# Optimization experiments

Measured on AMD Instinct MI355X. Metric: run time of the kernel, lower is better.

The kernel has to match this reference:

```python
import math
import jax, jax.numpy as jnp
import numpy as np

HEAD_DIM = 64

def setup_inputs() -> dict:
    key = jax.random.key(0)
    kq, kk, kv = jax.random.split(key, 3)
    B, S, D = 16, 2048, HEAD_DIM
    q = jax.random.normal(kq, (B, S, D), dtype=jnp.float32)
    k = jax.random.normal(kk, (B, S, D), dtype=jnp.float32)
    v = jax.random.normal(kv, (B, S, D), dtype=jnp.float32)
    return {"q": q, "k": k, "v": v}

def reference(q, k, v):
    # scores: [B, Sq, Sk]
    scores = jnp.einsum('bqd,bkd->bqk', q, k) / math.sqrt(HEAD_DIM)
    # NOTE: original uses nn.Softmax(dim=1) -> softmax over the QUERY axis
    weights = jax.nn.softmax(scores, axis=1)
    # dropout p=0.0 -> identity
    return jnp.einsum('bqk,bkd->bqd', weights, v)
```

## Files before the change

kernel.cpp:

```cpp
#include <hip/hip_runtime.h>
#include <hip/hip_bf16.h>

#define S_LEN 2048
#define D_DIM 64
#define NB 16

#define C_EXP 0.1803368801111204f

typedef __attribute__((ext_vector_type(8))) __bf16 bf16x8;
typedef __attribute__((ext_vector_type(4))) __bf16 bf16x4;
typedef __attribute__((ext_vector_type(4))) float f32x4;

#define GLOAD16(gp, lp)                                              \
  __builtin_amdgcn_global_load_lds(                                  \
      (const __attribute__((address_space(1))) void*)(gp),           \
      (__attribute__((address_space(3))) void*)(lp), 16, 0, 0)

__global__ __launch_bounds__(256) void convert_bf16_kernel(
    const float* __restrict__ qf, const float* __restrict__ kf,
    __bf16* __restrict__ qb, __bf16* __restrict__ kb) {
  const int n4 = NB * S_LEN * D_DIM / 4;
  for (int i = blockIdx.x * blockDim.x + threadIdx.x; i < n4;
       i += gridDim.x * blockDim.x) {
    float4 a = ((const float4*)qf)[i];
    float4 c = ((const float4*)kf)[i];
    bf16x4 oa = {(__bf16)a.x, (__bf16)a.y, (__bf16)a.z, (__bf16)a.w};
    bf16x4 oc = {(__bf16)c.x, (__bf16)c.y, (__bf16)c.z, (__bf16)c.w};
    ((bf16x4*)qb)[i] = oa;
    ((bf16x4*)kb)[i] = oc;
  }
}

__global__ __launch_bounds__(256) void stats_kernel(
    const __bf16* __restrict__ Qb, const __bf16* __restrict__ Kb,
    float* __restrict__ Lpart, int qlen) {
  __shared__ __align__(16) __bf16 QT[4096];
  const int b = blockIdx.y;
  const int kblk = blockIdx.x;
  const int qs = blockIdx.z;
  const int tid = threadIdx.x;
  const int wave = tid >> 6;
  const int lane = tid & 63;
  const int l16 = lane & 15;
  const int g = lane >> 4;

  const int kbase = kblk * 64 + wave * 16;
  const __bf16* kp = Kb + ((size_t)b * S_LEN + kbase + l16) * D_DIM + g * 8;
  bf16x8 ak0 = *(const bf16x8*)(kp);
  bf16x8 ak1 = *(const bf16x8*)(kp + 32);

  const int srow = tid >> 3;
  const int scol = 8 * ((tid & 7) ^ (srow & 7));

  float sacc[4] = {0.f, 0.f, 0.f, 0.f};
  const __bf16* Qbase = Qb + (size_t)b * S_LEN * D_DIM;
  const int qbeg = qs * qlen;

  for (int q0 = qbeg; q0 < qbeg + qlen; q0 += 64) {
    __syncthreads();
#pragma unroll
    for (int h = 0; h < 2; ++h)
      GLOAD16(Qbase + (size_t)(q0 + h * 32 + srow) * D_DIM + scol,
              (char*)QT + h * 4096 + (size_t)tid * 16);
    asm volatile("s_waitcnt vmcnt(0)" ::: "memory");
    __syncthreads();

#pragma unroll
    for (int qt = 0; qt < 4; ++qt) {
      const int r = qt * 16 + l16;
      bf16x8 bq0 = *(const bf16x8*)(QT + r * 64 + 8 * (g ^ (r & 7)));
      bf16x8 bq1 = *(const bf16x8*)(QT + r * 64 + 8 * ((g + 4) ^ (r & 7)));
      f32x4 t = __builtin_amdgcn_mfma_f32_16x16x32_bf16(
          ak0, bq0, (f32x4){0.f, 0.f, 0.f, 0.f}, 0, 0, 0);
      t = __builtin_amdgcn_mfma_f32_16x16x32_bf16(ak1, bq1, t, 0, 0, 0);
#pragma unroll
      for (int r4 = 0; r4 < 4; ++r4)
        sacc[r4] += __builtin_amdgcn_exp2f(t[r4] * C_EXP);
    }
  }
#pragma unroll
  for (int r4 = 0; r4 < 4; ++r4) {
    float v = sacc[r4];
    v += __shfl_xor(v, 1);
    v += __shfl_xor(v, 2);
    v += __shfl_xor(v, 4);
    v += __shfl_xor(v, 8);
    if (l16 == 0)
      Lpart[(size_t)qs * NB * S_LEN + (size_t)b * S_LEN + kbase + g * 4 + r4] =
          v;
  }
}

__global__ __launch_bounds__(256) void scalev_kernel(
    const float* __restrict__ V, const float* __restrict__ Lpart,
    __bf16* __restrict__ Vt) {
  const int b = blockIdx.y;
  const int k = blockIdx.x * 256 + threadIdx.x;
  const size_t NS = (size_t)NB * S_LEN;
  const size_t idx = (size_t)b * S_LEN + k;
  const float L =
      Lpart[idx] + Lpart[NS + idx] + Lpart[2 * NS + idx] + Lpart[3 * NS + idx];
  const float inv = 1.0f / L;
  const float* vrow = V + ((size_t)b * S_LEN + k) * D_DIM;
  __bf16* vt = Vt + (size_t)b * D_DIM * S_LEN + k;
#pragma unroll
  for (int d = 0; d < D_DIM; ++d)
    vt[(size_t)d * S_LEN] = (__bf16)(vrow[d] * inv);
}

__global__ __launch_bounds__(256) void attn_out_kernel(
    const __bf16* __restrict__ Qb, const __bf16* __restrict__ Kb,
    const __bf16* __restrict__ Vt, float* __restrict__ Op, int klen) {
  __shared__ __align__(16) __bf16 KT[4096];
  __shared__ __align__(16) __bf16 VT[4096];
  __shared__ __align__(16) __bf16 Plds[4][16][72];
  const int b = blockIdx.y;
  const int qblk = blockIdx.x;
  const int ks = blockIdx.z;
  const int tid = threadIdx.x;
  const int wave = tid >> 6;
  const int lane = tid & 63;
  const int l16 = lane & 15;
  const int g = lane >> 4;

  const int qbase = qblk * 64 + wave * 16;
  const __bf16* qp = Qb + ((size_t)b * S_LEN + qbase + l16) * D_DIM + g * 8;
  bf16x8 aq0 = *(const bf16x8*)(qp);
  bf16x8 aq1 = *(const bf16x8*)(qp + 32);

  f32x4 acc[4] = {};
  const int srow = tid >> 3;
  const int scol = 8 * ((tid & 7) ^ (srow & 7));
  const __bf16* Kbase = Kb + (size_t)b * S_LEN * D_DIM;
  const __bf16* Vbase = Vt + (size_t)b * D_DIM * S_LEN;
  __bf16(*pl)[72] = Plds[wave];
  const int kbeg = ks * klen;

  for (int k0 = kbeg; k0 < kbeg + klen; k0 += 64) {
    __syncthreads();
#pragma unroll
    for (int h = 0; h < 2; ++h) {
      GLOAD16(Kbase + (size_t)(k0 + h * 32 + srow) * D_DIM + scol,
              (char*)KT + h * 4096 + (size_t)tid * 16);
      GLOAD16(Vbase + (size_t)(h * 32 + srow) * S_LEN + k0 + scol,
              (char*)VT + h * 4096 + (size_t)tid * 16);
    }
    asm volatile("s_waitcnt vmcnt(0)" ::: "memory");
    __syncthreads();

#pragma unroll
    for (int kt = 0; kt < 4; ++kt) {
      const int r = kt * 16 + l16;
      bf16x8 bk0 = *(const bf16x8*)(KT + r * 64 + 8 * (g ^ (r & 7)));
      bf16x8 bk1 = *(const bf16x8*)(KT + r * 64 + 8 * ((g + 4) ^ (r & 7)));
      f32x4 t = __builtin_amdgcn_mfma_f32_16x16x32_bf16(
          aq0, bk0, (f32x4){0.f, 0.f, 0.f, 0.f}, 0, 0, 0);
      t = __builtin_amdgcn_mfma_f32_16x16x32_bf16(aq1, bk1, t, 0, 0, 0);
#pragma unroll
      for (int r4 = 0; r4 < 4; ++r4)
        pl[g * 4 + r4][kt * 16 + l16] =
            (__bf16)__builtin_amdgcn_exp2f(t[r4] * C_EXP);
    }
    bf16x8 pa0 = *(const bf16x8*)(&pl[l16][g * 8]);
    bf16x8 pa1 = *(const bf16x8*)(&pl[l16][32 + g * 8]);
#pragma unroll
    for (int dt = 0; dt < 4; ++dt) {
      const int rd = dt * 16 + l16;
      bf16x8 bv0 = *(const bf16x8*)(VT + rd * 64 + 8 * (g ^ (rd & 7)));
      bf16x8 bv1 = *(const bf16x8*)(VT + rd * 64 + 8 * ((g + 4) ^ (rd & 7)));
      acc[dt] = __builtin_amdgcn_mfma_f32_16x16x32_bf16(pa0, bv0, acc[dt], 0, 0, 0);
      acc[dt] = __builtin_amdgcn_mfma_f32_16x16x32_bf16(pa1, bv1, acc[dt], 0, 0, 0);
    }
  }
  float* ob = Op + ((size_t)ks * NB + b) * (size_t)(S_LEN * D_DIM);
#pragma unroll
  for (int dt = 0; dt < 4; ++dt)
#pragma unroll
    for (int r4 = 0; r4 < 4; ++r4)
      ob[(size_t)(qbase + g * 4 + r4) * D_DIM + dt * 16 + l16] = acc[dt][r4];
}

__global__ __launch_bounds__(256) void reduce_kernel(
    const float* __restrict__ Op, float* __restrict__ out, int np) {
  const int i = blockIdx.x * 256 + threadIdx.x;
  const int slab = NB * S_LEN * D_DIM / 4;
  const float4* p = (const float4*)Op;
  float4 s = p[i];
  for (int j = 1; j < np; ++j) {
    float4 t = p[i + (size_t)j * slab];
    s.x += t.x; s.y += t.y; s.z += t.z; s.w += t.w;
  }
  ((float4*)out)[i] = s;
}

extern "C" void kernel_launch(void* const* d_in, const int* in_sizes, int n_in,
                              void* d_out, int out_size, void* d_ws,
                              size_t ws_size, hipStream_t stream) {
  const float* q = (const float*)d_in[0];
  const float* k = (const float*)d_in[1];
  const float* v = (const float*)d_in[2];
  float* out = (float*)d_out;

  char* ws = (char*)d_ws;
  const size_t nelem = (size_t)NB * S_LEN * D_DIM;
  __bf16* Qb = (__bf16*)ws;
  __bf16* Kb = (__bf16*)(ws + nelem * 2);
  __bf16* Vt = (__bf16*)(ws + nelem * 4);
  float* Lp = (float*)(ws + nelem * 6);
  float* Op = (float*)(ws + (13u << 20));

  int ksplit = 1;
  if (ws_size >= (13u << 20) + 4 * nelem * 4) ksplit = 4;
  else if (ws_size >= (13u << 20) + 2 * nelem * 4) ksplit = 2;

  convert_bf16_kernel<<<1024, 256, 0, stream>>>(q, k, Qb, Kb);
  stats_kernel<<<dim3(32, 16, 4), 256, 0, stream>>>(Qb, Kb, Lp, S_LEN / 4);
  scalev_kernel<<<dim3(8, 16), 256, 0, stream>>>(v, Lp, Vt);
  float* attn_dst = (ksplit == 1) ? out : Op;
  attn_out_kernel<<<dim3(32, 16, ksplit), 256, 0, stream>>>(Qb, Kb, Vt,
                                                            attn_dst,
                                                            S_LEN / ksplit);
  if (ksplit > 1)
    reduce_kernel<<<(int)(nelem / 4 / 256), 256, 0, stream>>>(Op, out, ksplit);
}
```

Measured before the change: 134.5 us.

## Load Q/K/V MFMA operands directly from global memory instead of LDS staging

Removes the LDS staging of Q tiles in the stats kernel and K/V tiles in the attention kernel. Each wave now fetches its MFMA B-operands straight from global memory with 16-byte vector loads, which drops the block-wide barriers and the async global-to-LDS copies. The cost is that the four waves of a block each fetch the same K/V/Q data, relying on L1/L2 to absorb the repeats, and load latency is no longer hidden behind an explicit staged tile.

Result: slower. 261.3 us (+94.3%).

```diff
diff --git a/kernel.cpp b/kernel.cpp
--- a/kernel.cpp
+++ b/kernel.cpp
@@ -10,11 +10,6 @@
 typedef __attribute__((ext_vector_type(8))) __bf16 bf16x8;
 typedef __attribute__((ext_vector_type(4))) __bf16 bf16x4;
 typedef __attribute__((ext_vector_type(4))) float f32x4;
-
-#define GLOAD16(gp, lp)                                              \
-  __builtin_amdgcn_global_load_lds(                                  \
-      (const __attribute__((address_space(1))) void*)(gp),           \
-      (__attribute__((address_space(3))) void*)(lp), 16, 0, 0)
 
 __global__ __launch_bounds__(256) void convert_bf16_kernel(
     const float* __restrict__ qf, const float* __restrict__ kf,
@@ -34,13 +29,11 @@
 __global__ __launch_bounds__(256) void stats_kernel(
     const __bf16* __restrict__ Qb, const __bf16* __restrict__ Kb,
     float* __restrict__ Lpart, int qlen) {
-  __shared__ __align__(16) __bf16 QT[4096];
   const int b = blockIdx.y;
   const int kblk = blockIdx.x;
   const int qs = blockIdx.z;
-  const int tid = threadIdx.x;
-  const int wave = tid >> 6;
-  const int lane = tid & 63;
+  const int wave = threadIdx.x >> 6;
+  const int lane = threadIdx.x & 63;
   const int l16 = lane & 15;
   const int g = lane >> 4;
 
@@ -49,27 +42,16 @@
   bf16x8 ak0 = *(const bf16x8*)(kp);
   bf16x8 ak1 = *(const bf16x8*)(kp + 32);
 
-  const int srow = tid >> 3;
-  const int scol = 8 * ((tid & 7) ^ (srow & 7));
-
   float sacc[4] = {0.f, 0.f, 0.f, 0.f};
   const __bf16* Qbase = Qb + (size_t)b * S_LEN * D_DIM;
   const int qbeg = qs * qlen;
 
   for (int q0 = qbeg; q0 < qbeg + qlen; q0 += 64) {
-    __syncthreads();
-#pragma unroll
-    for (int h = 0; h < 2; ++h)
-      GLOAD16(Qbase + (size_t)(q0 + h * 32 + srow) * D_DIM + scol,
-              (char*)QT + h * 4096 + (size_t)tid * 16);
-    asm volatile("s_waitcnt vmcnt(0)" ::: "memory");
-    __syncthreads();
-
 #pragma unroll
     for (int qt = 0; qt < 4; ++qt) {
-      const int r = qt * 16 + l16;
-      bf16x8 bq0 = *(const bf16x8*)(QT + r * 64 + 8 * (g ^ (r & 7)));
-      bf16x8 bq1 = *(const bf16x8*)(QT + r * 64 + 8 * ((g + 4) ^ (r & 7)));
+      const __bf16* qp = Qbase + (size_t)(q0 + qt * 16 + l16) * D_DIM + g * 8;
+      bf16x8 bq0 = *(const bf16x8*)(qp);
+      bf16x8 bq1 = *(const bf16x8*)(qp + 32);
       f32x4 t = __builtin_amdgcn_mfma_f32_16x16x32_bf16(
           ak0, bq0, (f32x4){0.f, 0.f, 0.f, 0.f}, 0, 0, 0);
       t = __builtin_amdgcn_mfma_f32_16x16x32_bf16(ak1, bq1, t, 0, 0, 0);
@@ -111,15 +93,12 @@
 __global__ __launch_bounds__(256) void attn_out_kernel(
     const __bf16* __restrict__ Qb, const __bf16* __restrict__ Kb,
     const __bf16* __restrict__ Vt, float* __restrict__ Op, int klen) {
-  __shared__ __align__(16) __bf16 KT[4096];
-  __shared__ __align__(16) __bf16 VT[4096];
   __shared__ __align__(16) __bf16 Plds[4][16][72];
   const int b = blockIdx.y;
   const int qblk = blockIdx.x;
   const int ks = blockIdx.z;
-  const int tid = threadIdx.x;
-  const int wave = tid >> 6;
-  const int lane = tid & 63;
+  const int wave = threadIdx.x >> 6;
+  const int lane = threadIdx.x & 63;
   const int l16 = lane & 15;
   const int g = lane >> 4;
 
@@ -129,30 +108,17 @@
   bf16x8 aq1 = *(const bf16x8*)(qp + 32);
 
   f32x4 acc[4] = {};
-  const int srow = tid >> 3;
-  const int scol = 8 * ((tid & 7) ^ (srow & 7));
   const __bf16* Kbase = Kb + (size_t)b * S_LEN * D_DIM;
   const __bf16* Vbase = Vt + (size_t)b * D_DIM * S_LEN;
   __bf16(*pl)[72] = Plds[wave];
   const int kbeg = ks * klen;
 
   for (int k0 = kbeg; k0 < kbeg + klen; k0 += 64) {
-    __syncthreads();
-#pragma unroll
-    for (int h = 0; h < 2; ++h) {
-      GLOAD16(Kbase + (size_t)(k0 + h * 32 + srow) * D_DIM + scol,
-              (char*)KT + h * 4096 + (size_t)tid * 16);
-      GLOAD16(Vbase + (size_t)(h * 32 + srow) * S_LEN + k0 + scol,
-              (char*)VT + h * 4096 + (size_t)tid * 16);
-    }
-    asm volatile("s_waitcnt vmcnt(0)" ::: "memory");
-    __syncthreads();
-
 #pragma unroll
     for (int kt = 0; kt < 4; ++kt) {
-      const int r = kt * 16 + l16;
-      bf16x8 bk0 = *(const bf16x8*)(KT + r * 64 + 8 * (g ^ (r & 7)));
-      bf16x8 bk1 = *(const bf16x8*)(KT + r * 64 + 8 * ((g + 4) ^ (r & 7)));
+      const __bf16* kp = Kbase + (size_t)(k0 + kt * 16 + l16) * D_DIM + g * 8;
+      bf16x8 bk0 = *(const bf16x8*)(kp);
+      bf16x8 bk1 = *(const bf16x8*)(kp + 32);
       f32x4 t = __builtin_amdgcn_mfma_f32_16x16x32_bf16(
           aq0, bk0, (f32x4){0.f, 0.f, 0.f, 0.f}, 0, 0, 0);
       t = __builtin_amdgcn_mfma_f32_16x16x32_bf16(aq1, bk1, t, 0, 0, 0);
@@ -165,9 +131,9 @@
     bf16x8 pa1 = *(const bf16x8*)(&pl[l16][32 + g * 8]);
 #pragma unroll
     for (int dt = 0; dt < 4; ++dt) {
-      const int rd = dt * 16 + l16;
-      bf16x8 bv0 = *(const bf16x8*)(VT + rd * 64 + 8 * (g ^ (rd & 7)));
-      bf16x8 bv1 = *(const bf16x8*)(VT + rd * 64 + 8 * ((g + 4) ^ (rd & 7)));
+      const __bf16* vp = Vbase + (size_t)(dt * 16 + l16) * S_LEN + k0 + g * 8;
+      bf16x8 bv0 = *(const bf16x8*)(vp);
+      bf16x8 bv1 = *(const bf16x8*)(vp + 32);
       acc[dt] = __builtin_amdgcn_mfma_f32_16x16x32_bf16(pa0, bv0, acc[dt], 0, 0, 0);
       acc[dt] = __builtin_amdgcn_mfma_f32_16x16x32_bf16(pa1, bv1, acc[dt], 0, 0, 0);
     }
```
